# Performance work log

Measured on AMD Instinct MI355X. Metric: run time of the kernel, lower is better.

## Reference

```python
import jax, jax.numpy as jnp
import numpy as np

D_K = 64

def setup_inputs() -> dict:
    key = jax.random.key(0)
    ks = jax.random.split(key, 9)
    B, S, D = 8, 2048, 512
    d_k, d_v = 64, 64
    return {
        "q_in": jax.random.normal(ks[0], (B, S, D), jnp.float32),
        "k_in": jax.random.normal(ks[1], (B, S, D), jnp.float32),
        "v_in": jax.random.normal(ks[2], (B, S, D), jnp.float32),
        "Wq": jax.random.normal(ks[3], (D, d_k), jnp.float32) * 0.05,
        "bq": jax.random.normal(ks[4], (d_k,), jnp.float32) * 0.05,
        "Wk": jax.random.normal(ks[5], (D, d_k), jnp.float32) * 0.05,
        "bk": jax.random.normal(ks[6], (d_k,), jnp.float32) * 0.05,
        "Wv": jax.random.normal(ks[7], (D, d_v), jnp.float32) * 0.05,
        "bv": jax.random.normal(ks[8], (d_v,), jnp.float32) * 0.05,
    }

def reference(q_in, k_in, v_in, Wq, bq, Wk, bk, Wv, bv):
    # Dense projections: x @ W + b
    q = jnp.einsum('bsd,dk->bsk', q_in, Wq) + bq  # [B,S,d_k]
    k = jnp.einsum('bsd,dk->bsk', k_in, Wk) + bk  # [B,S,d_k]
    v = jnp.einsum('bsd,dv->bsv', v_in, Wv) + bv  # [B,S,d_v]
    scale = 1.0 / np.sqrt(D_K).astype(np.float32)
    scores = jnp.einsum('bqk,bsk->bqs', q, k) * scale  # [B,S,S]
    attn = jax.nn.softmax(scores, axis=-1)
    return jnp.einsum('bqs,bsv->bqv', attn, v)  # [B,S,d_v]
```

## Files before the change

kernel.cpp:

```cpp
#include <hip/hip_runtime.h>
#include <hip/hip_bf16.h>
#include <cstdint>

typedef __attribute__((ext_vector_type(8))) short short8;
typedef __attribute__((ext_vector_type(16))) float f32x16;

#if __has_builtin(__builtin_amdgcn_exp2f)
#define EXP2F(x) __builtin_amdgcn_exp2f(x)
#else
#define EXP2F(x) exp2f(x)
#endif

#define MFMA32(A, B, C) __builtin_amdgcn_mfma_f32_32x32x16_bf16((A), (B), (C), 0, 0, 0)

__device__ __forceinline__ unsigned short f2bf(float f) {
  unsigned int u = __builtin_bit_cast(unsigned int, f);
  u += 0x7FFFu + ((u >> 16) & 1u);
  return (unsigned short)(u >> 16);
}

__global__ __launch_bounds__(256) void prep_wt(
    const float* __restrict__ Wq, const float* __restrict__ Wk,
    const float* __restrict__ Wv, unsigned short* __restrict__ Wt)
{
  int idx = blockIdx.x * 256 + threadIdx.x;
  int which = idx >> 15;
  int rem = idx & 32767;
  int n = rem >> 9;
  int k = rem & 511;
  const float* W = (which == 0) ? Wq : (which == 1) ? Wk : Wv;
  Wt[idx] = f2bf(W[k * 64 + n]);
}

__global__ __launch_bounds__(256) void proj_qk(
    const float* __restrict__ qin, const float* __restrict__ kin,
    const unsigned short* __restrict__ Wt,
    const float* __restrict__ bq, const float* __restrict__ bk,
    unsigned short* __restrict__ Qo, unsigned short* __restrict__ Ko)
{
  const int which = blockIdx.y;
  const float* X    = which ? kin : qin;
  const float* bias = which ? bk  : bq;
  unsigned short* Y = which ? Ko  : Qo;
  const unsigned short* wt = Wt + (size_t)which * 64 * 512;

  const int lane = threadIdx.x & 63;
  const int wave = threadIdx.x >> 6;
  const int h = lane >> 5, l31 = lane & 31;
  const int rowbase = blockIdx.x * 128 + wave * 32;
  const float* xrow = X + (size_t)(rowbase + l31) * 512 + h * 8;
  const unsigned short* w0 = wt + (size_t)l31 * 512 + h * 8;
  const unsigned short* w1 = w0 + 32 * 512;

  f32x16 acc0 = {}, acc1 = {};
  #pragma unroll 4
  for (int kc = 0; kc < 32; ++kc) {
    float4 a0 = *(const float4*)(xrow + kc * 16);
    float4 a1 = *(const float4*)(xrow + kc * 16 + 4);
    short8 af = { (short)f2bf(a0.x), (short)f2bf(a0.y), (short)f2bf(a0.z), (short)f2bf(a0.w),
                  (short)f2bf(a1.x), (short)f2bf(a1.y), (short)f2bf(a1.z), (short)f2bf(a1.w) };
    short8 b0 = *(const short8*)(w0 + kc * 16);
    short8 b1 = *(const short8*)(w1 + kc * 16);
    acc0 = MFMA32(af, b0, acc0);
    acc1 = MFMA32(af, b1, acc1);
  }

  const float scale = which ? 1.0f : 0.18033688f;
  const float bias0 = bias[l31], bias1 = bias[l31 + 32];
  #pragma unroll
  for (int r = 0; r < 16; ++r) {
    int row = (r & 3) + 8 * (r >> 2) + 4 * h;
    size_t base = (size_t)(rowbase + row) * 64;
    Y[base + l31]      = f2bf((acc0[r] + bias0) * scale);
    Y[base + l31 + 32] = f2bf((acc1[r] + bias1) * scale);
  }
}

__global__ __launch_bounds__(256) void proj_v(
    const float* __restrict__ vin, const unsigned short* __restrict__ Wt,
    const float* __restrict__ bv, unsigned short* __restrict__ Vto)
{
  __shared__ unsigned short TB[64 * 140];

  const int lane = threadIdx.x & 63;
  const int wave = threadIdx.x >> 6;
  const int h = lane >> 5, l31 = lane & 31;
  const int rowbase = blockIdx.x * 128 + wave * 32;
  const float* xrow = vin + (size_t)(rowbase + l31) * 512 + h * 8;
  const unsigned short* wt = Wt + (size_t)2 * 64 * 512;
  const unsigned short* w0 = wt + (size_t)l31 * 512 + h * 8;
  const unsigned short* w1 = w0 + 32 * 512;

  f32x16 acc0 = {}, acc1 = {};
  #pragma unroll 4
  for (int kc = 0; kc < 32; ++kc) {
    float4 a0 = *(const float4*)(xrow + kc * 16);
    float4 a1 = *(const float4*)(xrow + kc * 16 + 4);
    short8 af = { (short)f2bf(a0.x), (short)f2bf(a0.y), (short)f2bf(a0.z), (short)f2bf(a0.w),
                  (short)f2bf(a1.x), (short)f2bf(a1.y), (short)f2bf(a1.z), (short)f2bf(a1.w) };
    short8 b0 = *(const short8*)(w0 + kc * 16);
    short8 b1 = *(const short8*)(w1 + kc * 16);
    acc0 = MFMA32(af, b0, acc0);
    acc1 = MFMA32(af, b1, acc1);
  }

  const float bias0 = bv[l31], bias1 = bv[l31 + 32];
  #pragma unroll
  for (int r = 0; r < 16; ++r) {
    int row = (r & 3) + 8 * (r >> 2) + 4 * h;
    int sl = wave * 32 + row;
    TB[l31 * 140 + sl]        = f2bf(acc0[r] + bias0);
    TB[(l31 + 32) * 140 + sl] = f2bf(acc1[r] + bias1);
  }
  __syncthreads();
  int bidx = blockIdx.x >> 4;
  int s0 = (blockIdx.x & 15) * 128;
  for (int i = threadIdx.x; i < 64 * 32; i += 256) {
    int n = i >> 5, c = i & 31;
    ushort4 v4 = *(const ushort4*)(TB + n * 140 + c * 4);
    *(ushort4*)(Vto + ((size_t)bidx * 64 + n) * 2048 + s0 + c * 4) = v4;
  }
}

__global__ __launch_bounds__(512, 2) void attn_kernel(
    const unsigned short* __restrict__ Q, const unsigned short* __restrict__ K,
    const unsigned short* __restrict__ Vt, float* __restrict__ out)
{
  __shared__ float ObS[4][16][64];
  __shared__ float MpS[4][64];
  __shared__ float LpS[4][64];

  const int tid = threadIdx.x;
  const int lane = tid & 63, w = tid >> 6;
  const int h = lane >> 5, l31 = lane & 31;
  const int b = blockIdx.y;
  const int q0 = blockIdx.x * 64;

  short8 qf[2][4];
  #pragma unroll
  for (int qt = 0; qt < 2; ++qt) {
    const unsigned short* qp = Q + ((size_t)(b * 2048 + q0 + qt * 32 + l31)) * 64 + h * 8;
    #pragma unroll
    for (int c = 0; c < 4; ++c) qf[qt][c] = *(const short8*)(qp + c * 16);
  }

  f32x16 o00 = {}, o01 = {}, o10 = {}, o11 = {};
  float m0 = -1e30f, m1 = -1e30f, ls0 = 0.f, ls1 = 0.f;

  for (int st = 0; st < 8; ++st) {
    const int kb = w * 256 + st * 32;
    short8 kf[4];
    const unsigned short* kp = K + ((size_t)(b * 2048 + kb + l31)) * 64 + h * 8;
    #pragma unroll
    for (int c = 0; c < 4; ++c) kf[c] = *(const short8*)(kp + c * 16);
    short8 vf0[2], vf1[2];
    {
      const unsigned short* vp0 = Vt + ((size_t)(b * 64 + l31)) * 2048 + kb + h * 8;
      const unsigned short* vp1 = Vt + ((size_t)(b * 64 + 32 + l31)) * 2048 + kb + h * 8;
      vf0[0] = *(const short8*)(vp0);  vf0[1] = *(const short8*)(vp0 + 16);
      vf1[0] = *(const short8*)(vp1);  vf1[1] = *(const short8*)(vp1 + 16);
    }
    #pragma unroll
    for (int qt = 0; qt < 2; ++qt) {
      f32x16 sT = {};
      #pragma unroll
      for (int c = 0; c < 4; ++c) sT = MFMA32(kf[c], qf[qt][c], sT);
      float mx = sT[0];
      #pragma unroll
      for (int r = 1; r < 16; ++r) mx = fmaxf(mx, sT[r]);
      mx = fmaxf(mx, __shfl_xor(mx, 32, 64));
      float mold = qt ? m1 : m0;
      float mnew = fmaxf(mold, mx);
      float alpha = EXP2F(mold - mnew);
      float rs = 0.f;
      float p[16];
      #pragma unroll
      for (int r = 0; r < 16; ++r) { p[r] = EXP2F(sT[r] - mnew); rs += p[r]; }
      rs += __shfl_xor(rs, 32, 64);
      unsigned int pk[8];
      #pragma unroll
      for (int i = 0; i < 8; ++i)
        pk[i] = (unsigned int)f2bf(p[2 * i]) | ((unsigned int)f2bf(p[2 * i + 1]) << 16);
      unsigned int ex[8];
      #pragma unroll
      for (int i = 0; i < 8; ++i) ex[i] = (unsigned int)__shfl_xor((int)pk[i], 32, 64);
      uint4 cc0, cc1;
      if (h == 0) { cc0 = make_uint4(pk[0], pk[1], ex[0], ex[1]); cc1 = make_uint4(pk[4], pk[5], ex[4], ex[5]); }
      else        { cc0 = make_uint4(ex[2], ex[3], pk[2], pk[3]); cc1 = make_uint4(ex[6], ex[7], pk[6], pk[7]); }
      short8 P0 = __builtin_bit_cast(short8, cc0);
      short8 P1 = __builtin_bit_cast(short8, cc1);
      if (qt == 0) {
        m0 = mnew; ls0 = ls0 * alpha + rs;
        o00 *= alpha; o10 *= alpha;
        o00 = MFMA32(vf0[0], P0, o00); o00 = MFMA32(vf0[1], P1, o00);
        o10 = MFMA32(vf1[0], P0, o10); o10 = MFMA32(vf1[1], P1, o10);
      } else {
        m1 = mnew; ls1 = ls1 * alpha + rs;
        o01 *= alpha; o11 *= alpha;
        o01 = MFMA32(vf0[0], P0, o01); o01 = MFMA32(vf0[1], P1, o01);
        o11 = MFMA32(vf1[0], P0, o11); o11 = MFMA32(vf1[1], P1, o11);
      }
    }
  }

  for (int half = 4; half > 0; half >>= 1) {
    const bool writer = (w >= half) && (w < 2 * half);
    const bool merger = (w < half);
    __syncthreads();
    if (writer && h == 0) {
      MpS[w - half][l31] = m0;      LpS[w - half][l31] = ls0;
      MpS[w - half][32 + l31] = m1; LpS[w - half][32 + l31] = ls1;
    }
    __syncthreads();
    float fb0 = 0.f, fb1 = 0.f;
    if (merger) {
      float pm0 = MpS[w][l31],      pl0 = LpS[w][l31];
      float pm1 = MpS[w][32 + l31], pl1 = LpS[w][32 + l31];
      float nm0 = fmaxf(m0, pm0), nm1 = fmaxf(m1, pm1);
      float fa0 = EXP2F(m0 - nm0); fb0 = EXP2F(pm0 - nm0);
      float fa1 = EXP2F(m1 - nm1); fb1 = EXP2F(pm1 - nm1);
      m0 = nm0; m1 = nm1;
      ls0 = ls0 * fa0 + pl0 * fb0; ls1 = ls1 * fa1 + pl1 * fb1;
      o00 *= fa0; o10 *= fa0; o01 *= fa1; o11 *= fa1;
    }
    __syncthreads();
    if (writer) {
      #pragma unroll
      for (int r = 0; r < 16; ++r) ObS[w - half][r][lane] = o00[r]; }
    __syncthreads();
    if (merger) {
      #pragma unroll
      for (int r = 0; r < 16; ++r) o00[r] += ObS[w][r][lane] * fb0; }
    __syncthreads();
    if (writer) {
      #pragma unroll
      for (int r = 0; r < 16; ++r) ObS[w - half][r][lane] = o01[r]; }
    __syncthreads();
    if (merger) {
      #pragma unroll
      for (int r = 0; r < 16; ++r) o01[r] += ObS[w][r][lane] * fb1; }
    __syncthreads();
    if (writer) {
      #pragma unroll
      for (int r = 0; r < 16; ++r) ObS[w - half][r][lane] = o10[r]; }
    __syncthreads();
    if (merger) {
      #pragma unroll
      for (int r = 0; r < 16; ++r) o10[r] += ObS[w][r][lane] * fb0; }
    __syncthreads();
    if (writer) {
      #pragma unroll
      for (int r = 0; r < 16; ++r) ObS[w - half][r][lane] = o11[r]; }
    __syncthreads();
    if (merger) {
      #pragma unroll
      for (int r = 0; r < 16; ++r) o11[r] += ObS[w][r][lane] * fb1; }
  }

  if (w == 0) {
    float i0 = 1.0f / ls0, i1 = 1.0f / ls1;
    o00 *= i0; o10 *= i0; o01 *= i1; o11 *= i1;
    #pragma unroll
    for (int qt = 0; qt < 2; ++qt) {
      int q = qt * 32 + l31;
      float* ob = out + ((size_t)(b * 2048 + q0 + q)) * 64 + 4 * h;
      const f32x16 a = qt ? o01 : o00;
      const f32x16 c = qt ? o11 : o10;
      #pragma unroll
      for (int g = 0; g < 4; ++g) {
        *(float4*)(ob + 8 * g)      = make_float4(a[4*g], a[4*g+1], a[4*g+2], a[4*g+3]);
        *(float4*)(ob + 32 + 8 * g) = make_float4(c[4*g], c[4*g+1], c[4*g+2], c[4*g+3]);
      }
    }
  }
}

extern "C" void kernel_launch(void* const* d_in, const int* in_sizes, int n_in,
                              void* d_out, int out_size, void* d_ws, size_t ws_size,
                              hipStream_t stream) {
  const float* qin = (const float*)d_in[0];
  const float* kin = (const float*)d_in[1];
  const float* vin = (const float*)d_in[2];
  const float* Wq  = (const float*)d_in[3];
  const float* bq  = (const float*)d_in[4];
  const float* Wk  = (const float*)d_in[5];
  const float* bk  = (const float*)d_in[6];
  const float* Wv  = (const float*)d_in[7];
  const float* bv  = (const float*)d_in[8];

  unsigned short* Qo  = (unsigned short*)d_ws;
  unsigned short* Ko  = Qo + (size_t)16384 * 64;
  unsigned short* Vto = Ko + (size_t)16384 * 64;
  unsigned short* Wt  = Vto + (size_t)8 * 64 * 2048;
  float* out = (float*)d_out;

  hipLaunchKernelGGL(prep_wt, dim3(384), dim3(256), 0, stream, Wq, Wk, Wv, Wt);
  hipLaunchKernelGGL(proj_qk, dim3(128, 2), dim3(256), 0, stream,
                     qin, kin, Wt, bq, bk, Qo, Ko);
  hipLaunchKernelGGL(proj_v, dim3(128), dim3(256), 0, stream, vin, Wt, bv, Vto);
  hipLaunchKernelGGL(attn_kernel, dim3(32, 8), dim3(512), 0, stream, Qo, Ko, Vto, out);
}
```

Measured before the change: 186.9 us.

## Merge QKV projections into one launch with split-K across waves

Combines the Q/K and V projection kernels into a single launch over a 256x3 grid. Each block now covers 64 rows, with the reduction dimension split between wave pairs and the partial sums combined through shared memory. The aim is to remove one kernel launch and raise the number of blocks so the fp32 input reads spread across more CUs. In exchange it adds an LDS reduction and extra barriers, and half the waves sit idle during the epilogue.

Result: faster. 171.5 us (-8.2%).

```diff
diff --git a/kernel.cpp b/kernel.cpp
--- a/kernel.cpp
+++ b/kernel.cpp
@@ -32,29 +32,37 @@
   Wt[idx] = f2bf(W[k * 64 + n]);
 }
 
-__global__ __launch_bounds__(256) void proj_qk(
+__global__ __launch_bounds__(256, 3) void proj_kernel(
     const float* __restrict__ qin, const float* __restrict__ kin,
-    const unsigned short* __restrict__ Wt,
+    const float* __restrict__ vin, const unsigned short* __restrict__ Wt,
     const float* __restrict__ bq, const float* __restrict__ bk,
-    unsigned short* __restrict__ Qo, unsigned short* __restrict__ Ko)
+    const float* __restrict__ bv,
+    unsigned short* __restrict__ Qo, unsigned short* __restrict__ Ko,
+    unsigned short* __restrict__ Vto)
 {
+  __shared__ char smem_raw[16384];
+  float* red = (float*)smem_raw;
+  unsigned short* TB = (unsigned short*)smem_raw;
+
   const int which = blockIdx.y;
-  const float* X    = which ? kin : qin;
-  const float* bias = which ? bk  : bq;
-  unsigned short* Y = which ? Ko  : Qo;
-  const unsigned short* wt = Wt + (size_t)which * 64 * 512;
+  const float* X    = (which == 0) ? qin : (which == 1) ? kin : vin;
+  const float* bias = (which == 0) ? bq  : (which == 1) ? bk  : bv;
 
   const int lane = threadIdx.x & 63;
-  const int wave = threadIdx.x >> 6;
+  const int wv = threadIdx.x >> 6;
   const int h = lane >> 5, l31 = lane & 31;
-  const int rowbase = blockIdx.x * 128 + wave * 32;
-  const float* xrow = X + (size_t)(rowbase + l31) * 512 + h * 8;
-  const unsigned short* w0 = wt + (size_t)l31 * 512 + h * 8;
+  const int grp = wv & 1;
+  const int kh = wv >> 1;
+  const int rowbase = blockIdx.x * 64 + grp * 32;
+
+  const float* xrow = X + (size_t)(rowbase + l31) * 512 + kh * 256 + h * 8;
+  const unsigned short* wbase = Wt + (size_t)which * 64 * 512 + kh * 256 + h * 8;
+  const unsigned short* w0 = wbase + (size_t)l31 * 512;
   const unsigned short* w1 = w0 + 32 * 512;
 
   f32x16 acc0 = {}, acc1 = {};
   #pragma unroll 4
-  for (int kc = 0; kc < 32; ++kc) {
+  for (int kc = 0; kc < 16; ++kc) {
     float4 a0 = *(const float4*)(xrow + kc * 16);
     float4 a1 = *(const float4*)(xrow + kc * 16 + 4);
     short8 af = { (short)f2bf(a0.x), (short)f2bf(a0.y), (short)f2bf(a0.z), (short)f2bf(a0.w),
@@ -65,60 +73,57 @@
     acc1 = MFMA32(af, b1, acc1);
   }
 
-  const float scale = which ? 1.0f : 0.18033688f;
+  if (kh == 1) {
+    #pragma unroll
+    for (int r = 0; r < 16; ++r) {
+      int row = (r & 3) + 8 * (r >> 2) + 4 * h;
+      red[grp * 2048 + row * 64 + l31]      = acc0[r];
+      red[grp * 2048 + row * 64 + l31 + 32] = acc1[r];
+    }
+  }
+  __syncthreads();
+  if (kh == 0) {
+    #pragma unroll
+    for (int r = 0; r < 16; ++r) {
+      int row = (r & 3) + 8 * (r >> 2) + 4 * h;
+      acc0[r] += red[grp * 2048 + row * 64 + l31];
+      acc1[r] += red[grp * 2048 + row * 64 + l31 + 32];
+    }
+  }
+
   const float bias0 = bias[l31], bias1 = bias[l31 + 32];
-  #pragma unroll
-  for (int r = 0; r < 16; ++r) {
-    int row = (r & 3) + 8 * (r >> 2) + 4 * h;
-    size_t base = (size_t)(rowbase + row) * 64;
-    Y[base + l31]      = f2bf((acc0[r] + bias0) * scale);
-    Y[base + l31 + 32] = f2bf((acc1[r] + bias1) * scale);
-  }
-}
-
-__global__ __launch_bounds__(256) void proj_v(
-    const float* __restrict__ vin, const unsigned short* __restrict__ Wt,
-    const float* __restrict__ bv, unsigned short* __restrict__ Vto)
-{
-  __shared__ unsigned short TB[64 * 140];
-
-  const int lane = threadIdx.x & 63;
-  const int wave = threadIdx.x >> 6;
-  const int h = lane >> 5, l31 = lane & 31;
-  const int rowbase = blockIdx.x * 128 + wave * 32;
-  const float* xrow = vin + (size_t)(rowbase + l31) * 512 + h * 8;
-  const unsigned short* wt = Wt + (size_t)2 * 64 * 512;
-  const unsigned short* w0 = wt + (size_t)l31 * 512 + h * 8;
-  const unsigned short* w1 = w0 + 32 * 512;
-
-  f32x16 acc0 = {}, acc1 = {};
-  #pragma unroll 4
-  for (int kc = 0; kc < 32; ++kc) {
-    float4 a0 = *(const float4*)(xrow + kc * 16);
-    float4 a1 = *(const float4*)(xrow + kc * 16 + 4);
-    short8 af = { (short)f2bf(a0.x), (short)f2bf(a0.y), (short)f2bf(a0.z), (short)f2bf(a0.w),
-                  (short)f2bf(a1.x), (short)f2bf(a1.y), (short)f2bf(a1.z), (short)f2bf(a1.w) };
-    short8 b0 = *(const short8*)(w0 + kc * 16);
-    short8 b1 = *(const short8*)(w1 + kc * 16);
-    acc0 = MFMA32(af, b0, acc0);
-    acc1 = MFMA32(af, b1, acc1);
-  }
-
-  const float bias0 = bv[l31], bias1 = bv[l31 + 32];
-  #pragma unroll
-  for (int r = 0; r < 16; ++r) {
-    int row = (r & 3) + 8 * (r >> 2) + 4 * h;
-    int sl = wave * 32 + row;
-    TB[l31 * 140 + sl]        = f2bf(acc0[r] + bias0);
-    TB[(l31 + 32) * 140 + sl] = f2bf(acc1[r] + bias1);
-  }
-  __syncthreads();
-  int bidx = blockIdx.x >> 4;
-  int s0 = (blockIdx.x & 15) * 128;
-  for (int i = threadIdx.x; i < 64 * 32; i += 256) {
-    int n = i >> 5, c = i & 31;
-    ushort4 v4 = *(const ushort4*)(TB + n * 140 + c * 4);
-    *(ushort4*)(Vto + ((size_t)bidx * 64 + n) * 2048 + s0 + c * 4) = v4;
+
+  if (which < 2) {
+    if (kh == 0) {
+      const float scale = which ? 1.0f : 0.18033688f;
+      unsigned short* Y = which ? Ko : Qo;
+      #pragma unroll
+      for (int r = 0; r < 16; ++r) {
+        int row = (r & 3) + 8 * (r >> 2) + 4 * h;
+        size_t base = (size_t)(rowbase + row) * 64;
+        Y[base + l31]      = f2bf((acc0[r] + bias0) * scale);
+        Y[base + l31 + 32] = f2bf((acc1[r] + bias1) * scale);
+      }
+    }
+  } else {
+    __syncthreads();
+    if (kh == 0) {
+      #pragma unroll
+      for (int r = 0; r < 16; ++r) {
+        int row = (r & 3) + 8 * (r >> 2) + 4 * h;
+        int sl = grp * 32 + row;
+        TB[l31 * 68 + sl]        = f2bf(acc0[r] + bias0);
+        TB[(l31 + 32) * 68 + sl] = f2bf(acc1[r] + bias1);
+      }
+    }
+    __syncthreads();
+    int bidx = blockIdx.x >> 5;
+    int s0 = (blockIdx.x & 31) * 64;
+    for (int i = threadIdx.x; i < 64 * 16; i += 256) {
+      int n = i >> 4, c = i & 15;
+      ushort4 v4 = *(const ushort4*)(TB + n * 68 + c * 4);
+      *(ushort4*)(Vto + ((size_t)bidx * 64 + n) * 2048 + s0 + c * 4) = v4;
+    }
   }
 }
 
@@ -295,8 +300,7 @@
   float* out = (float*)d_out;
 
   hipLaunchKernelGGL(prep_wt, dim3(384), dim3(256), 0, stream, Wq, Wk, Wv, Wt);
-  hipLaunchKernelGGL(proj_qk, dim3(128, 2), dim3(256), 0, stream,
-                     qin, kin, Wt, bq, bk, Qo, Ko);
-  hipLaunchKernelGGL(proj_v, dim3(128), dim3(256), 0, stream, vin, Wt, bv, Vto);
+  hipLaunchKernelGGL(proj_kernel, dim3(256, 3), dim3(256), 0, stream,
+                     qin, kin, vin, Wt, bq, bk, bv, Qo, Ko, Vto);
   hipLaunchKernelGGL(attn_kernel, dim3(32, 8), dim3(512), 0, stream, Qo, Ko, Vto, out);
 }
```
